# Kernel tuning notes

Hardware: AMD Instinct MI355X
Metric: run time of the kernel (lower is better)

Reference implementation:

```python
import jax, jax.numpy as jnp
import numpy as np

# init kwargs (constants of the module)
SF = 0.05          # quantization scale factor
GROUP_SIZE = 8     # values per group sharing a term budget
NUM_EXPS = 12      # max number of power-of-two terms kept per group
MAXBITS = 8        # bit-width of the quantized integer magnitude


def setup_inputs() -> dict:
    key = jax.random.key(0)
    x = jax.random.normal(key, (4096, 4096), dtype=jnp.float32)
    return {"x": x}


def _radix2_mod_group(x):
    qmax = 2 ** MAXBITS - 1
    # uniform quantization to signed integers
    q = jnp.clip(jnp.round(x / SF), -qmax, qmax).astype(jnp.int32)
    sign = jnp.sign(q)
    mag = jnp.abs(q)
    g = mag.reshape(-1, GROUP_SIZE)                       # [G, gs]
    exps = jnp.arange(MAXBITS, dtype=jnp.int32)           # [B]
    bits = (g[..., None] >> exps) & 1                     # [G, gs, B] radix-2 terms
    # candidate terms: exponent where the bit is set, -1 otherwise
    cand = jnp.where(bits == 1, exps, -1).reshape(-1, GROUP_SIZE * MAXBITS)
    # keep the NUM_EXPS largest-exponent terms in each group (ties -> lowest index)
    _, idx = jax.lax.top_k(cand, NUM_EXPS)                # [G, NUM_EXPS]
    gidx = jnp.arange(cand.shape[0])[:, None]
    keep = jnp.zeros_like(cand).at[gidx, idx].set(1)      # [G, gs*B]
    keep = keep.reshape(-1, GROUP_SIZE, MAXBITS) * bits   # mask out slots with no term
    recon = jnp.sum(keep << exps, axis=-1)                # [G, gs] kept-term magnitude
    recon = recon * sign.reshape(-1, GROUP_SIZE)
    return (recon.astype(x.dtype) * jnp.asarray(SF, x.dtype)).reshape(x.shape)


def reference(x):
    return _radix2_mod_group(x)
```

## Files before the change

kernel.cpp:

```cpp
#include <hip/hip_runtime.h>


constexpr float SF = 0.05f;
constexpr int GS = 8;
constexpr int NUM_EXPS = 12;
constexpr int MAXBITS = 8;
constexpr float QMAXF = 255.0f;

__global__ __launch_bounds__(256) void radix2_mod_group_kernel(
    const float* __restrict__ x, float* __restrict__ out, int ngroups) {
  int g = blockIdx.x * blockDim.x + threadIdx.x;
  if (g >= ngroups) return;

  const float4* __restrict__ xv = reinterpret_cast<const float4*>(x);
  float4 a = xv[2 * g];
  float4 b = xv[2 * g + 1];
  float v[GS] = {a.x, a.y, a.z, a.w, b.x, b.y, b.z, b.w};

  int mag[GS];
  int neg[GS];
#pragma unroll
  for (int i = 0; i < GS; ++i) {
    float r = rintf(v[i] / SF);
    r = fminf(fmaxf(r, -QMAXF), QMAXF);
    int q = (int)r;
    neg[i] = (q < 0);
    mag[i] = neg[i] ? -q : q;
  }

  int budget = NUM_EXPS;
  unsigned keepm[GS] = {0, 0, 0, 0, 0, 0, 0, 0};
#pragma unroll
  for (int e = MAXBITS - 1; e >= 0; --e) {
    unsigned m = 0;
#pragma unroll
    for (int i = 0; i < GS; ++i) m |= (((unsigned)mag[i] >> e) & 1u) << i;
    int cnt = __popc(m);
    unsigned kept;
    if (cnt <= budget) {
      kept = m;
      budget -= cnt;
    } else {
      kept = 0u;
      unsigned mm = m;
      for (int k = 0; k < budget; ++k) {
        kept |= mm & (0u - mm);
        mm &= mm - 1u;
      }
      budget = 0;
    }
#pragma unroll
    for (int i = 0; i < GS; ++i) keepm[i] |= ((kept >> i) & 1u) << e;
  }

  float o[GS];
#pragma unroll
  for (int i = 0; i < GS; ++i) {
    int r = mag[i] & (int)keepm[i];
    float f = (float)r * SF;
    o[i] = neg[i] ? -f : f;
  }

  float4* __restrict__ ov = reinterpret_cast<float4*>(out);
  ov[2 * g] = make_float4(o[0], o[1], o[2], o[3]);
  ov[2 * g + 1] = make_float4(o[4], o[5], o[6], o[7]);
}

extern "C" void kernel_launch(void* const* d_in, const int* in_sizes, int n_in,
                              void* d_out, int out_size, void* d_ws, size_t ws_size,
                              hipStream_t stream) {
  const float* x = (const float*)d_in[0];
  float* out = (float*)d_out;
  int n = in_sizes[0];
  int ngroups = n / GS;
  int block = 256;
  int grid = (ngroups + block - 1) / block;
  radix2_mod_group_kernel<<<grid, block, 0, stream>>>(x, out, ngroups);
}
```

Baseline: 120.0 us.

## Replace per-exponent budget loop with 8x8 bit-matrix transpose and rank select

Packs the eight 8-bit magnitudes into a 64-bit word and transposes it so the bits are ordered by exponent, then by element. A single popcount plus a binary-search select finds the cutoff position that keeps the top twelve terms. A second transpose turns the kept mask back into per-element magnitudes, and the sign is restored with copysign from the input. This removes the data-dependent branchy loop over exponents and lanes. The risk is that it needs the exact bit ordering to reproduce the tie-breaking, and signed zero may differ slightly when the output is zero.

```diff
diff --git a/kernel.cpp b/kernel.cpp
--- a/kernel.cpp
+++ b/kernel.cpp
@@ -2,66 +2,67 @@
 
 
 constexpr float SF = 0.05f;
-constexpr int GS = 8;
 constexpr int NUM_EXPS = 12;
-constexpr int MAXBITS = 8;
-constexpr float QMAXF = 255.0f;
+
+__device__ __forceinline__ unsigned long long transpose8x8(unsigned long long x) {
+  unsigned long long t;
+  t = (x ^ (x >> 7)) & 0x00AA00AA00AA00AAull; x ^= t ^ (t << 7);
+  t = (x ^ (x >> 14)) & 0x0000CCCC0000CCCCull; x ^= t ^ (t << 14);
+  t = (x ^ (x >> 28)) & 0x00000000F0F0F0F0ull; x ^= t ^ (t << 28);
+  return x;
+}
 
 __global__ __launch_bounds__(256) void radix2_mod_group_kernel(
-    const float* __restrict__ x, float* __restrict__ out, int ngroups) {
+    const float4* __restrict__ xv, float4* __restrict__ ov, int ngroups) {
   int g = blockIdx.x * blockDim.x + threadIdx.x;
   if (g >= ngroups) return;
 
-  const float4* __restrict__ xv = reinterpret_cast<const float4*>(x);
   float4 a = xv[2 * g];
   float4 b = xv[2 * g + 1];
-  float v[GS] = {a.x, a.y, a.z, a.w, b.x, b.y, b.z, b.w};
+  float v[8] = {a.x, a.y, a.z, a.w, b.x, b.y, b.z, b.w};
 
-  int mag[GS];
-  int neg[GS];
+  unsigned long long M = 0ull;
 #pragma unroll
-  for (int i = 0; i < GS; ++i) {
+  for (int i = 0; i < 8; ++i) {
     float r = rintf(v[i] / SF);
-    r = fminf(fmaxf(r, -QMAXF), QMAXF);
-    int q = (int)r;
-    neg[i] = (q < 0);
-    mag[i] = neg[i] ? -q : q;
+    r = fminf(fmaxf(r, -255.0f), 255.0f);
+    int qi = (int)r;
+    unsigned mi = (unsigned)(qi < 0 ? -qi : qi);
+    M |= (unsigned long long)mi << (8 * (7 - i));
   }
 
-  int budget = NUM_EXPS;
-  unsigned keepm[GS] = {0, 0, 0, 0, 0, 0, 0, 0};
+  unsigned long long w = transpose8x8(M);
+
+  int P = __popcll(w);
+  int j = P > NUM_EXPS ? P - NUM_EXPS : 0;
+
+  unsigned long long xx = w;
+  int pos = 0;
+  int c;
+  c = __popcll(xx & 0xffffffffull);
+  { int t = (j >= c); pos += t << 5; j -= t ? c : 0; xx = t ? (xx >> 32) : xx; }
+  c = __popc((unsigned)xx & 0xffffu);
+  { int t = (j >= c); pos += t << 4; j -= t ? c : 0; xx = t ? (xx >> 16) : xx; }
+  c = __popc((unsigned)xx & 0xffu);
+  { int t = (j >= c); pos += t << 3; j -= t ? c : 0; xx = t ? (xx >> 8) : xx; }
+  c = __popc((unsigned)xx & 0xfu);
+  { int t = (j >= c); pos += t << 2; j -= t ? c : 0; xx = t ? (xx >> 4) : xx; }
+  c = __popc((unsigned)xx & 0x3u);
+  { int t = (j >= c); pos += t << 1; j -= t ? c : 0; xx = t ? (xx >> 2) : xx; }
+  c = (int)((unsigned)xx & 1u);
+  { int t = (j >= c); pos += t; }
+
+  unsigned long long keep = w & (~0ull << pos);
+
+  unsigned long long Kt = transpose8x8(keep);
+
+  float o[8];
 #pragma unroll
-  for (int e = MAXBITS - 1; e >= 0; --e) {
-    unsigned m = 0;
-#pragma unroll
-    for (int i = 0; i < GS; ++i) m |= (((unsigned)mag[i] >> e) & 1u) << i;
-    int cnt = __popc(m);
-    unsigned kept;
-    if (cnt <= budget) {
-      kept = m;
-      budget -= cnt;
-    } else {
-      kept = 0u;
-      unsigned mm = m;
-      for (int k = 0; k < budget; ++k) {
-        kept |= mm & (0u - mm);
-        mm &= mm - 1u;
-      }
-      budget = 0;
-    }
-#pragma unroll
-    for (int i = 0; i < GS; ++i) keepm[i] |= ((kept >> i) & 1u) << e;
+  for (int i = 0; i < 8; ++i) {
+    unsigned mi = (unsigned)(Kt >> (8 * (7 - i))) & 0xffu;
+    o[i] = copysignf((float)mi * SF, v[i]);
   }
 
-  float o[GS];
-#pragma unroll
-  for (int i = 0; i < GS; ++i) {
-    int r = mag[i] & (int)keepm[i];
-    float f = (float)r * SF;
-    o[i] = neg[i] ? -f : f;
-  }
-
-  float4* __restrict__ ov = reinterpret_cast<float4*>(out);
   ov[2 * g] = make_float4(o[0], o[1], o[2], o[3]);
   ov[2 * g + 1] = make_float4(o[4], o[5], o[6], o[7]);
 }
@@ -72,8 +73,9 @@
   const float* x = (const float*)d_in[0];
   float* out = (float*)d_out;
   int n = in_sizes[0];
-  int ngroups = n / GS;
+  int ngroups = n / 8;
   int block = 256;
   int grid = (ngroups + block - 1) / block;
-  radix2_mod_group_kernel<<<grid, block, 0, stream>>>(x, out, ngroups);
+  radix2_mod_group_kernel<<<grid, block, 0, stream>>>(
+      (const float4*)x, (float4*)out, ngroups);
 }
```

Result: faster. 111.9 us (-6.7%).
